# Optimization experiments

Hardware: AMD Instinct MI355X
Metric: run time of the kernel (lower is better)

## Reference

```python
import jax, jax.numpy as jnp
import numpy as np

B, S, H, E, TOP_K = 4, 4096, 4096, 64, 2

def setup_inputs() -> dict:
    key = jax.random.key(0)
    k1, k2 = jax.random.split(key)
    hidden_states = jax.random.normal(k1, (B, S, H), dtype=jnp.float32)
    gate_weight = jax.random.normal(k2, (E, H), dtype=jnp.float32) * (H ** -0.5)
    return {"hidden_states": hidden_states, "gate_weight": gate_weight}

def reference(hidden_states, gate_weight):
    # gate: logits[b,s,e] = hidden[b,s,h] @ W[e,h]^T (nn.Linear, no bias)
    router_logits = jnp.einsum('bsh,eh->bse', hidden_states, gate_weight)
    router_probs = jax.nn.softmax(router_logits, axis=-1)
    # top-k over experts, then renormalize the selected weights
    expert_weights, expert_indices = jax.lax.top_k(router_probs, TOP_K)
    expert_weights = expert_weights / jnp.sum(expert_weights, axis=-1, keepdims=True)
    return (router_probs, expert_indices, expert_weights)
```

## Files before the change

### kernel.cpp

```cpp
#include <hip/hip_runtime.h>
#include <math.h>

#define TOKENS 16384
#define HDIM 4096
#define NE 64

#define BM 64
#define BK 32
#define KSPLIT 8
#define KSLICE (HDIM / KSPLIT)
#define LDSP 68

__global__ __launch_bounds__(256, 4) void router_gemm(const float* __restrict__ A,
                                                      const float* __restrict__ W,
                                                      float* __restrict__ P) {
  __shared__ float As[BK * LDSP];
  __shared__ float Ws[BK * LDSP];

  const int tid = threadIdx.x;
  const int bt = blockIdx.x;
  const int ks = blockIdx.y;

  const int sr = tid >> 2;
  const int sc = (tid & 3) * 4;

  const float* Ab = A + (size_t)(bt * BM + sr) * HDIM + (size_t)ks * KSLICE + sc;
  const float* Wb = W + (size_t)sr * HDIM + (size_t)ks * KSLICE + sc;

  const int tx = tid & 15;
  const int ty = tid >> 4;

  float acc[4][4];
#pragma unroll
  for (int i = 0; i < 4; ++i)
#pragma unroll
    for (int j = 0; j < 4; ++j) acc[i][j] = 0.f;

  float4 a0 = *(const float4*)(Ab);
  float4 a1 = *(const float4*)(Ab + 16);
  float4 w0 = *(const float4*)(Wb);
  float4 w1 = *(const float4*)(Wb + 16);

  for (int kc = 0; kc < KSLICE; kc += BK) {
    As[(sc + 0) * LDSP + sr] = a0.x;
    As[(sc + 1) * LDSP + sr] = a0.y;
    As[(sc + 2) * LDSP + sr] = a0.z;
    As[(sc + 3) * LDSP + sr] = a0.w;
    As[(sc + 16) * LDSP + sr] = a1.x;
    As[(sc + 17) * LDSP + sr] = a1.y;
    As[(sc + 18) * LDSP + sr] = a1.z;
    As[(sc + 19) * LDSP + sr] = a1.w;
    Ws[(sc + 0) * LDSP + sr] = w0.x;
    Ws[(sc + 1) * LDSP + sr] = w0.y;
    Ws[(sc + 2) * LDSP + sr] = w0.z;
    Ws[(sc + 3) * LDSP + sr] = w0.w;
    Ws[(sc + 16) * LDSP + sr] = w1.x;
    Ws[(sc + 17) * LDSP + sr] = w1.y;
    Ws[(sc + 18) * LDSP + sr] = w1.z;
    Ws[(sc + 19) * LDSP + sr] = w1.w;
    __syncthreads();

    if (kc + BK < KSLICE) {
      a0 = *(const float4*)(Ab + kc + BK);
      a1 = *(const float4*)(Ab + kc + BK + 16);
      w0 = *(const float4*)(Wb + kc + BK);
      w1 = *(const float4*)(Wb + kc + BK + 16);
    }

#pragma unroll
    for (int k = 0; k < BK; ++k) {
      float4 av = *(const float4*)&As[k * LDSP + ty * 4];
      float4 wv = *(const float4*)&Ws[k * LDSP + tx * 4];
      const float a[4] = {av.x, av.y, av.z, av.w};
      const float w[4] = {wv.x, wv.y, wv.z, wv.w};
#pragma unroll
      for (int i = 0; i < 4; ++i)
#pragma unroll
        for (int j = 0; j < 4; ++j) acc[i][j] = fmaf(a[i], w[j], acc[i][j]);
    }
    __syncthreads();
  }

  float* Pb = P + ((size_t)ks * TOKENS + (size_t)bt * BM + ty * 4) * NE + tx * 4;
#pragma unroll
  for (int i = 0; i < 4; ++i)
    *(float4*)(Pb + (size_t)i * NE) =
        make_float4(acc[i][0], acc[i][1], acc[i][2], acc[i][3]);
}

__global__ __launch_bounds__(256) void router_finalize(const float* __restrict__ P,
                                                       float* __restrict__ out) {
  const int lane = threadIdx.x & 63;
  const int wave = threadIdx.x >> 6;
  const int tok = blockIdx.x * 4 + wave;

  float l = 0.f;
#pragma unroll
  for (int s = 0; s < KSPLIT; ++s)
    l += P[((size_t)s * TOKENS + tok) * NE + lane];

  float m = l;
#pragma unroll
  for (int off = 32; off >= 1; off >>= 1) m = fmaxf(m, __shfl_xor(m, off, 64));

  const float e = expf(l - m);
  float sum = e;
#pragma unroll
  for (int off = 32; off >= 1; off >>= 1) sum += __shfl_xor(sum, off, 64);

  const float p = e / sum;
  out[(size_t)tok * NE + lane] = p;

  float m0 = p;
#pragma unroll
  for (int off = 32; off >= 1; off >>= 1) m0 = fmaxf(m0, __shfl_xor(m0, off, 64));
  const unsigned long long b0 = __ballot(p == m0);
  const int i0 = __ffsll(b0) - 1;

  const float pm = (lane == i0) ? -1.f : p;
  float m1 = pm;
#pragma unroll
  for (int off = 32; off >= 1; off >>= 1) m1 = fmaxf(m1, __shfl_xor(m1, off, 64));
  const unsigned long long b1 = __ballot(pm == m1);
  const int i1 = __ffsll(b1) - 1;

  if (lane == 0) {
    float* idxo = out + (size_t)TOKENS * NE + (size_t)tok * 2;
    idxo[0] = (float)i0;
    idxo[1] = (float)i1;
    float* wo = out + (size_t)TOKENS * NE + (size_t)TOKENS * 2 + (size_t)tok * 2;
    const float d = m0 + m1;
    wo[0] = m0 / d;
    wo[1] = m1 / d;
  }
}

extern "C" void kernel_launch(void* const* d_in, const int* in_sizes, int n_in,
                              void* d_out, int out_size, void* d_ws, size_t ws_size,
                              hipStream_t stream) {
  const float* A = (const float*)d_in[0];
  const float* W = (const float*)d_in[1];
  float* out = (float*)d_out;
  float* P = (float*)d_ws;

  dim3 gridA(TOKENS / BM, KSPLIT);
  router_gemm<<<gridA, 256, 0, stream>>>(A, W, P);
  router_finalize<<<TOKENS / 4, 256, 0, stream>>>(P, out);
}
```

Before: 399.4 us.

## Enlarge router GEMM tile to 256 tokens with 8x8 register microtiles

Raises the token tile from 64 to 256 and gives each thread an 8x8 accumulator block instead of 4x4, which doubles arithmetic per shared-memory load and reuses each expert-weight tile across more tokens. BK drops to 16 and KSPLIT doubles to 16 so grid size stays high. The costs are 64 accumulators per thread, which may hurt occupancy under launch_bounds(256,4) or cause spills, and twice as many partial-sum slices for the finalize kernel to read. The finalize kernel still sums only KSPLIT slices, so it picks up the new count automatically, but the workspace must be large enough for 16 slices.

```diff
diff --git a/kernel.cpp b/kernel.cpp
--- a/kernel.cpp
+++ b/kernel.cpp
@@ -5,87 +5,87 @@
 #define HDIM 4096
 #define NE 64
 
-#define BM 64
-#define BK 32
-#define KSPLIT 8
+#define BM 256
+#define BK 16
+#define KSPLIT 16
 #define KSLICE (HDIM / KSPLIT)
-#define LDSP 68
+#define LDA 260
+#define LDW 68
 
 __global__ __launch_bounds__(256, 4) void router_gemm(const float* __restrict__ A,
                                                       const float* __restrict__ W,
                                                       float* __restrict__ P) {
-  __shared__ float As[BK * LDSP];
-  __shared__ float Ws[BK * LDSP];
+  __shared__ float As[BK * LDA];
+  __shared__ float Ws[BK * LDW];
 
   const int tid = threadIdx.x;
   const int bt = blockIdx.x;
   const int ks = blockIdx.y;
 
-  const int sr = tid >> 2;
-  const int sc = (tid & 3) * 4;
+  const int stok = tid >> 2;
+  const int sk = (tid & 3) * 4;
+  const float* Ab = A + (size_t)(bt * BM + stok) * HDIM + (size_t)ks * KSLICE + sk;
+  const float* Wb = W + (size_t)stok * HDIM + (size_t)ks * KSLICE + sk;
 
-  const float* Ab = A + (size_t)(bt * BM + sr) * HDIM + (size_t)ks * KSLICE + sc;
-  const float* Wb = W + (size_t)sr * HDIM + (size_t)ks * KSLICE + sc;
+  const int tx = tid & 7;
+  const int ty = tid >> 3;
 
-  const int tx = tid & 15;
-  const int ty = tid >> 4;
+  float acc[8][8];
+#pragma unroll
+  for (int i = 0; i < 8; ++i)
+#pragma unroll
+    for (int j = 0; j < 8; ++j) acc[i][j] = 0.f;
 
-  float acc[4][4];
+  float4 pa[4], pw;
 #pragma unroll
-  for (int i = 0; i < 4; ++i)
-#pragma unroll
-    for (int j = 0; j < 4; ++j) acc[i][j] = 0.f;
-
-  float4 a0 = *(const float4*)(Ab);
-  float4 a1 = *(const float4*)(Ab + 16);
-  float4 w0 = *(const float4*)(Wb);
-  float4 w1 = *(const float4*)(Wb + 16);
+  for (int i = 0; i < 4; ++i) pa[i] = *(const float4*)(Ab + (size_t)i * 64 * HDIM);
+  pw = *(const float4*)(Wb);
 
   for (int kc = 0; kc < KSLICE; kc += BK) {
-    As[(sc + 0) * LDSP + sr] = a0.x;
-    As[(sc + 1) * LDSP + sr] = a0.y;
-    As[(sc + 2) * LDSP + sr] = a0.z;
-    As[(sc + 3) * LDSP + sr] = a0.w;
-    As[(sc + 16) * LDSP + sr] = a1.x;
-    As[(sc + 17) * LDSP + sr] = a1.y;
-    As[(sc + 18) * LDSP + sr] = a1.z;
-    As[(sc + 19) * LDSP + sr] = a1.w;
-    Ws[(sc + 0) * LDSP + sr] = w0.x;
-    Ws[(sc + 1) * LDSP + sr] = w0.y;
-    Ws[(sc + 2) * LDSP + sr] = w0.z;
-    Ws[(sc + 3) * LDSP + sr] = w0.w;
-    Ws[(sc + 16) * LDSP + sr] = w1.x;
-    Ws[(sc + 17) * LDSP + sr] = w1.y;
-    Ws[(sc + 18) * LDSP + sr] = w1.z;
-    Ws[(sc + 19) * LDSP + sr] = w1.w;
+#pragma unroll
+    for (int i = 0; i < 4; ++i) {
+      const int col = stok + i * 64;
+      As[(sk + 0) * LDA + col] = pa[i].x;
+      As[(sk + 1) * LDA + col] = pa[i].y;
+      As[(sk + 2) * LDA + col] = pa[i].z;
+      As[(sk + 3) * LDA + col] = pa[i].w;
+    }
+    Ws[(sk + 0) * LDW + stok] = pw.x;
+    Ws[(sk + 1) * LDW + stok] = pw.y;
+    Ws[(sk + 2) * LDW + stok] = pw.z;
+    Ws[(sk + 3) * LDW + stok] = pw.w;
     __syncthreads();
 
     if (kc + BK < KSLICE) {
-      a0 = *(const float4*)(Ab + kc + BK);
-      a1 = *(const float4*)(Ab + kc + BK + 16);
-      w0 = *(const float4*)(Wb + kc + BK);
-      w1 = *(const float4*)(Wb + kc + BK + 16);
+#pragma unroll
+      for (int i = 0; i < 4; ++i)
+        pa[i] = *(const float4*)(Ab + (size_t)i * 64 * HDIM + kc + BK);
+      pw = *(const float4*)(Wb + kc + BK);
     }
 
 #pragma unroll
     for (int k = 0; k < BK; ++k) {
-      float4 av = *(const float4*)&As[k * LDSP + ty * 4];
-      float4 wv = *(const float4*)&Ws[k * LDSP + tx * 4];
-      const float a[4] = {av.x, av.y, av.z, av.w};
-      const float w[4] = {wv.x, wv.y, wv.z, wv.w};
+      float a[8], w[8];
+      *(float4*)&a[0] = *(const float4*)&As[k * LDA + ty * 8];
+      *(float4*)&a[4] = *(const float4*)&As[k * LDA + ty * 8 + 4];
+      *(float4*)&w[0] = *(const float4*)&Ws[k * LDW + tx * 8];
+      *(float4*)&w[4] = *(const float4*)&Ws[k * LDW + tx * 8 + 4];
 #pragma unroll
-      for (int i = 0; i < 4; ++i)
+      for (int i = 0; i < 8; ++i)
 #pragma unroll
-        for (int j = 0; j < 4; ++j) acc[i][j] = fmaf(a[i], w[j], acc[i][j]);
+        for (int j = 0; j < 8; ++j) acc[i][j] = fmaf(a[i], w[j], acc[i][j]);
     }
     __syncthreads();
   }
 
-  float* Pb = P + ((size_t)ks * TOKENS + (size_t)bt * BM + ty * 4) * NE + tx * 4;
+  float* Pb = P + ((size_t)ks * TOKENS + (size_t)bt * BM + ty * 8) * NE + tx * 8;
 #pragma unroll
-  for (int i = 0; i < 4; ++i)
+  for (int i = 0; i < 8; ++i) {
     *(float4*)(Pb + (size_t)i * NE) =
         make_float4(acc[i][0], acc[i][1], acc[i][2], acc[i][3]);
+    *(float4*)(Pb + (size_t)i * NE + 4) =
+        make_float4(acc[i][4], acc[i][5], acc[i][6], acc[i][7]);
+  }
 }
 
 __global__ __launch_bounds__(256) void router_finalize(const float* __restrict__ P,
```

Measured after the change: 929.5 us. 2.33x slower.

## Replace LDS-tiled router GEMM with per-lane expert, wave-uniform token loads

Applied to the files above, without the earlier changes.

Drops the shared-memory tiled GEMM. Each wave now handles 16 tokens and each lane computes one expert, reading its W row directly from global memory, while A rows are read with wave-uniform addresses that can become scalar loads. This removes LDS staging and barriers. In exchange, W reads become strided per lane, and A reuse depends on the scalar or L1 caches instead of shared memory.

```diff
diff --git a/kernel.cpp b/kernel.cpp
--- a/kernel.cpp
+++ b/kernel.cpp
@@ -5,87 +5,45 @@
 #define HDIM 4096
 #define NE 64
 
-#define BM 64
-#define BK 32
+#define TPW 16
 #define KSPLIT 8
 #define KSLICE (HDIM / KSPLIT)
-#define LDSP 68
 
-__global__ __launch_bounds__(256, 4) void router_gemm(const float* __restrict__ A,
-                                                      const float* __restrict__ W,
-                                                      float* __restrict__ P) {
-  __shared__ float As[BK * LDSP];
-  __shared__ float Ws[BK * LDSP];
+__global__ __launch_bounds__(256) void router_gemm(const float* __restrict__ A,
+                                                   const float* __restrict__ W,
+                                                   float* __restrict__ P) {
+  const int lane = threadIdx.x & 63;
+  const int wave = __builtin_amdgcn_readfirstlane(threadIdx.x >> 6);
+  const int tok0 = blockIdx.x * (4 * TPW) + wave * TPW;
+  const int kbeg = blockIdx.y * KSLICE;
 
-  const int tid = threadIdx.x;
-  const int bt = blockIdx.x;
-  const int ks = blockIdx.y;
+  const float* Arow = A + (size_t)tok0 * HDIM + kbeg;
+  const float* Wrow = W + (size_t)lane * HDIM + kbeg;
 
-  const int sr = tid >> 2;
-  const int sc = (tid & 3) * 4;
+  float acc[TPW];
+#pragma unroll
+  for (int t = 0; t < TPW; ++t) acc[t] = 0.f;
 
-  const float* Ab = A + (size_t)(bt * BM + sr) * HDIM + (size_t)ks * KSLICE + sc;
-  const float* Wb = W + (size_t)sr * HDIM + (size_t)ks * KSLICE + sc;
-
-  const int tx = tid & 15;
-  const int ty = tid >> 4;
-
-  float acc[4][4];
+  for (int kc = 0; kc < KSLICE; kc += 16) {
+    float4 w[4];
 #pragma unroll
-  for (int i = 0; i < 4; ++i)
+    for (int j = 0; j < 4; ++j) w[j] = *(const float4*)(Wrow + kc + j * 4);
 #pragma unroll
-    for (int j = 0; j < 4; ++j) acc[i][j] = 0.f;
-
-  float4 a0 = *(const float4*)(Ab);
-  float4 a1 = *(const float4*)(Ab + 16);
-  float4 w0 = *(const float4*)(Wb);
-  float4 w1 = *(const float4*)(Wb + 16);
-
-  for (int kc = 0; kc < KSLICE; kc += BK) {
-    As[(sc + 0) * LDSP + sr] = a0.x;
-    As[(sc + 1) * LDSP + sr] = a0.y;
-    As[(sc + 2) * LDSP + sr] = a0.z;
-    As[(sc + 3) * LDSP + sr] = a0.w;
-    As[(sc + 16) * LDSP + sr] = a1.x;
-    As[(sc + 17) * LDSP + sr] = a1.y;
-    As[(sc + 18) * LDSP + sr] = a1.z;
-    As[(sc + 19) * LDSP + sr] = a1.w;
-    Ws[(sc + 0) * LDSP + sr] = w0.x;
-    Ws[(sc + 1) * LDSP + sr] = w0.y;
-    Ws[(sc + 2) * LDSP + sr] = w0.z;
-    Ws[(sc + 3) * LDSP + sr] = w0.w;
-    Ws[(sc + 16) * LDSP + sr] = w1.x;
-    Ws[(sc + 17) * LDSP + sr] = w1.y;
-    Ws[(sc + 18) * LDSP + sr] = w1.z;
-    Ws[(sc + 19) * LDSP + sr] = w1.w;
-    __syncthreads();
-
-    if (kc + BK < KSLICE) {
-      a0 = *(const float4*)(Ab + kc + BK);
-      a1 = *(const float4*)(Ab + kc + BK + 16);
-      w0 = *(const float4*)(Wb + kc + BK);
-      w1 = *(const float4*)(Wb + kc + BK + 16);
+    for (int j = 0; j < 4; ++j) {
+#pragma unroll
+      for (int t = 0; t < TPW; ++t) {
+        float4 a = *(const float4*)(Arow + (size_t)t * HDIM + kc + j * 4);
+        acc[t] = fmaf(a.x, w[j].x, acc[t]);
+        acc[t] = fmaf(a.y, w[j].y, acc[t]);
+        acc[t] = fmaf(a.z, w[j].z, acc[t]);
+        acc[t] = fmaf(a.w, w[j].w, acc[t]);
+      }
     }
-
-#pragma unroll
-    for (int k = 0; k < BK; ++k) {
-      float4 av = *(const float4*)&As[k * LDSP + ty * 4];
-      float4 wv = *(const float4*)&Ws[k * LDSP + tx * 4];
-      const float a[4] = {av.x, av.y, av.z, av.w};
-      const float w[4] = {wv.x, wv.y, wv.z, wv.w};
-#pragma unroll
-      for (int i = 0; i < 4; ++i)
-#pragma unroll
-        for (int j = 0; j < 4; ++j) acc[i][j] = fmaf(a[i], w[j], acc[i][j]);
-    }
-    __syncthreads();
   }
 
-  float* Pb = P + ((size_t)ks * TOKENS + (size_t)bt * BM + ty * 4) * NE + tx * 4;
+  float* Pb = P + ((size_t)blockIdx.y * TOKENS + tok0) * NE + lane;
 #pragma unroll
-  for (int i = 0; i < 4; ++i)
-    *(float4*)(Pb + (size_t)i * NE) =
-        make_float4(acc[i][0], acc[i][1], acc[i][2], acc[i][3]);
+  for (int t = 0; t < TPW; ++t) Pb[(size_t)t * NE] = acc[t];
 }
 
 __global__ __launch_bounds__(256) void router_finalize(const float* __restrict__ P,
@@ -143,7 +101,7 @@
   float* out = (float*)d_out;
   float* P = (float*)d_ws;
 
-  dim3 gridA(TOKENS / BM, KSPLIT);
+  dim3 gridA(TOKENS / (4 * TPW), KSPLIT);
   router_gemm<<<gridA, 256, 0, stream>>>(A, W, P);
   router_finalize<<<TOKENS / 4, 256, 0, stream>>>(P, out);
 }
```

Measured after the change: 803.3 us. 101% more time.
